# Kernel optimization log

Measured on AMD Instinct MI355X. Metric: run time of the kernel, lower is better.

Reference implementation:

```python
import jax, jax.numpy as jnp
import numpy as np

N = 200_000   # nodes in batched graph
E = 400_000   # edges
D = 128       # embed_dim
L = 5         # num_layer
G = 1000      # number of graphs in batch
ATOM_V = 119  # atom vocab (OGB)
BOND_V = 5    # bond vocab (OGB)
OUT = 128     # output_dim
EPS = 1e-5


def setup_inputs() -> dict:
    key = jax.random.key(0)
    ks = jax.random.split(key, 16)
    inp = {
        "nfeat": jax.random.randint(ks[0], (N,), 0, ATOM_V),
        "efeat": jax.random.randint(ks[1], (E,), 0, BOND_V),
        "src": jax.random.randint(ks[2], (E,), 0, N),
        "dst": jax.random.randint(ks[3], (E,), 0, N),
        "node2graph": jnp.sort(jax.random.randint(ks[4], (N,), 0, G)),
        # learned parameters
        "atom_emb": jax.random.normal(ks[5], (ATOM_V, D), jnp.float32) * 0.02,
        "edge_emb": jax.random.normal(ks[6], (L, BOND_V, D), jnp.float32) * 0.02,
        "W": jax.random.normal(ks[7], (L, D, D), jnp.float32) * 0.02,
        "b": jnp.zeros((L, D), jnp.float32),
        "gamma": jnp.ones((L, D), jnp.float32),
        "beta": jnp.zeros((L, D), jnp.float32),
        "W1": jax.random.normal(ks[8], (D, D), jnp.float32) * 0.02,
        "b1": jnp.zeros((D,), jnp.float32),
        "W2": jax.random.normal(ks[9], (D, OUT), jnp.float32) * 0.02,
        "b2": jnp.zeros((OUT,), jnp.float32),
    }
    return inp


def reference(nfeat, efeat, src, dst, node2graph,
              atom_emb, edge_emb, W, b, gamma, beta, W1, b1, W2, b2):
    h = atom_emb[nfeat]                                  # [N, D]
    # in-degree + 1 (GCNConvLayer degree norm)
    deg = jax.ops.segment_sum(jnp.ones((E,), h.dtype), dst, num_segments=N) + 1.0
    for l in range(L):
        e = edge_emb[l][efeat]                           # [E, D] edge encoder
        m = h[src] + e                                   # u_add_e
        neigh = jax.ops.segment_sum(m, dst, num_segments=N)  # fn.sum -> 'neigh'
        h = ((h + neigh) / deg[:, None]) @ W[l] + b[l]   # project_node_feat
        # batch norm over nodes (training-mode batch stats), affine
        mu = jnp.mean(h, axis=0)
        var = jnp.var(h, axis=0)
        h = (h - mu) * jax.lax.rsqrt(var + EPS) * gamma[l] + beta[l]
        h = jax.nn.relu(h)                               # activation; dropout=eval
    # global mean pooling per graph
    cnt = jax.ops.segment_sum(jnp.ones((N,), h.dtype), node2graph, num_segments=G)
    g = jax.ops.segment_sum(h, node2graph, num_segments=G) / jnp.maximum(cnt, 1.0)[:, None]
    # predict MLP (dropout in eval mode = identity)
    out = jax.nn.relu(g @ W1 + b1) @ W2 + b2             # [G, OUT]
    return out
```

## Files before the change

### kernel.cpp

```cpp
#include <hip/hip_runtime.h>
#include <hip/hip_bf16.h>
#include <cstddef>

#define NN 200000
#define NE 400000
#define DD 128
#define NL 5
#define NG 1000
#define BOND_V 5
#define BM 32
#define NBLK (NN / BM)
#define MAXD 16
#define CHUNK 200
#define NB_SCAN 200
#define CH 1000
#define SB 125
#define EPS 1e-5f
#define XS 136

typedef __bf16 bf16x8 __attribute__((ext_vector_type(8)));
typedef float floatx4 __attribute__((ext_vector_type(4)));

__device__ __forceinline__ unsigned short f2bf(float f) {
    unsigned int u = __float_as_uint(f);
    u = (u + 0x7fffu + ((u >> 16) & 1u)) >> 16;
    return (unsigned short)u;
}
__device__ __forceinline__ float bf2f(unsigned short s) {
    return __uint_as_float(((unsigned int)s) << 16);
}
__device__ __forceinline__ float4 bf4_to_f4(uint2 v) {
    float4 o;
    o.x = __uint_as_float(v.x << 16);
    o.y = __uint_as_float(v.x & 0xffff0000u);
    o.z = __uint_as_float(v.y << 16);
    o.w = __uint_as_float(v.y & 0xffff0000u);
    return o;
}

__global__ void k_setup1(const int* __restrict__ dst, int* __restrict__ cnt,
                         const int* __restrict__ n2g, float* __restrict__ gcnt,
                         const float* __restrict__ W, unsigned short* __restrict__ Wht,
                         unsigned short* __restrict__ Wlt) {
    int e = blockIdx.x * blockDim.x + threadIdx.x;
    if (e < NE) atomicAdd(&cnt[dst[e]], 1);
    if (e < NN) atomicAdd(&gcnt[n2g[e]], 1.0f);
    if (e < NL * DD * DD) {
        int l = e / (DD * DD), rem = e % (DD * DD);
        int k = rem / DD, n = rem % DD;
        float v = W[e];
        unsigned short hb = f2bf(v);
        unsigned short lb = f2bf(v - bf2f(hb));
        size_t o = (size_t)l * DD * DD + (size_t)n * DD + k;
        Wht[o] = hb; Wlt[o] = lb;
    }
}

__global__ void k_scan1(const int* __restrict__ cnt, int* __restrict__ bsum) {
    __shared__ int sh[256];
    int b = blockIdx.x, t = threadIdx.x;
    int s = 0;
    if (t < CH / 4) {
        int base = b * CH + t * 4;
        s = cnt[base] + cnt[base + 1] + cnt[base + 2] + cnt[base + 3];
    }
    sh[t] = s;
    __syncthreads();
    if (t == 0) {
        int tot = 0;
        for (int i = 0; i < CH / 4; i++) tot += sh[i];
        bsum[b] = tot;
    }
}

__global__ void k_scan2(const int* __restrict__ bsum, int* __restrict__ bpre,
                        int* __restrict__ off) {
    if (threadIdx.x == 0) {
        int run = 0;
        for (int i = 0; i < NB_SCAN; i++) { bpre[i] = run; run += bsum[i]; }
        off[NN] = NE;
    }
}

__global__ void k_scan3(const int* __restrict__ cnt, const int* __restrict__ bpre,
                        int* __restrict__ off, int* __restrict__ cur,
                        float* __restrict__ rdeg) {
    __shared__ int sh[256];
    int b = blockIdx.x, t = threadIdx.x;
    int base = b * CH + t * 4;
    int c0 = 0, c1 = 0, c2 = 0, c3 = 0, s = 0;
    if (t < CH / 4) {
        c0 = cnt[base]; c1 = cnt[base + 1]; c2 = cnt[base + 2]; c3 = cnt[base + 3];
        s = c0 + c1 + c2 + c3;
    }
    sh[t] = s;
    __syncthreads();
    if (t == 0) {
        int run = bpre[b];
        for (int i = 0; i < CH / 4; i++) { int v = sh[i]; sh[i] = run; run += v; }
    }
    __syncthreads();
    if (t < CH / 4) {
        int run = sh[t];
        off[base] = run; cur[base] = run; run += c0;
        off[base + 1] = run; cur[base + 1] = run; run += c1;
        off[base + 2] = run; cur[base + 2] = run; run += c2;
        off[base + 3] = run; cur[base + 3] = run;
        rdeg[base]     = 1.0f / (float)(c0 + 1);
        rdeg[base + 1] = 1.0f / (float)(c1 + 1);
        rdeg[base + 2] = 1.0f / (float)(c2 + 1);
        rdeg[base + 3] = 1.0f / (float)(c3 + 1);
    }
}

__global__ void k_bucket(const int* __restrict__ src, const int* __restrict__ dst,
                         const int* __restrict__ efeat, int* __restrict__ cur,
                         int* __restrict__ esrc, int* __restrict__ eft) {
    int e = blockIdx.x * blockDim.x + threadIdx.x;
    if (e < NE) {
        int p = atomicAdd(&cur[dst[e]], 1);
        esrc[p] = src[e];
        eft[p] = efeat[e];
    }
}

__global__ void k_pad(const int* __restrict__ off, const int* __restrict__ esrc,
                      const int* __restrict__ eft, int* __restrict__ pent,
                      int* __restrict__ bperm, int* __restrict__ gmax) {
    __shared__ int offL[BM + 1];
    __shared__ int degS[BM];
    __shared__ int sortIdx[BM];
    __shared__ int gmaxS[8];
    int b = blockIdx.x, tid = threadIdx.x;
    if (tid <= BM) offL[tid] = off[b * BM + tid];
    __syncthreads();
    if (tid < BM) degS[tid] = offL[tid + 1] - offL[tid];
    __syncthreads();
    if (tid < BM) {
        int d = degS[tid], rank = 0;
        #pragma unroll
        for (int j = 0; j < BM; j++)
            rank += (degS[j] > d) || (degS[j] == d && j < tid);
        sortIdx[rank] = tid;
    }
    __syncthreads();
    if (tid < 8) {
        int g = degS[sortIdx[tid * 4]];
        gmaxS[tid] = g;
        gmax[b * 8 + tid] = g;
    }
    if (tid < BM) bperm[b * BM + tid] = sortIdx[tid];
    __syncthreads();
    for (int idx = tid; idx < BM * MAXD; idx += 256) {
        int p = idx & 31, j = idx >> 5, g = p >> 2;
        int gm = gmaxS[g]; if (gm > MAXD) gm = MAXD;
        if (j < gm) {
            int row = sortIdx[p];
            int d = degS[row];
            int v;
            if (j < d) { int e = offL[row] + j; v = esrc[e] | (eft[e] << 18); }
            else v = (5 << 18);
            pent[(size_t)b * MAXD * BM + j * BM + p] = v;
        }
    }
}

__device__ __forceinline__ float4 bnrelu4(float4 x, float4 m, float4 r, float4 g, float4 b) {
    float4 o;
    o.x = fmaxf(0.f, (x.x - m.x) * r.x * g.x + b.x);
    o.y = fmaxf(0.f, (x.y - m.y) * r.y * g.y + b.y);
    o.z = fmaxf(0.f, (x.z - m.z) * r.z * g.z + b.z);
    o.w = fmaxf(0.f, (x.w - m.w) * r.w * g.w + b.w);
    return o;
}

__global__ __launch_bounds__(256)
void k_fused(const void* __restrict__ basep, const int* __restrict__ nfeat, int first,
             const int* __restrict__ off, const int* __restrict__ esrc,
             const int* __restrict__ eft, const int* __restrict__ pent,
             const int* __restrict__ bperm, const int* __restrict__ gmax,
             const float* __restrict__ eemb, const float* __restrict__ rdeg,
             const float* __restrict__ muP, const float* __restrict__ rsP,
             const float* __restrict__ gamma, const float* __restrict__ beta,
             const unsigned short* __restrict__ Wht, const unsigned short* __restrict__ Wlt,
             const float* __restrict__ bias,
             unsigned short* __restrict__ C, float* __restrict__ part) {
    __shared__ unsigned short Xh[BM * XS];
    __shared__ unsigned short Xl[BM * XS];
    __shared__ float eS[6 * DD];
    __shared__ float red[4 * DD];
    __shared__ int offL[BM + 1];
    __shared__ int permL[BM];
    __shared__ int gmL[8];

    const float* baseF = (const float*)basep;
    const unsigned short* baseB = (const unsigned short*)basep;

    int tid = threadIdx.x;
    int n0 = blockIdx.x * BM;
    if (tid < 160) *(float4*)(eS + tid * 4) = *(const float4*)(eemb + tid * 4);
    else if (tid < 192) *(float4*)(eS + tid * 4) = (float4){0.f, 0.f, 0.f, 0.f};
    if (tid <= BM) offL[tid] = off[n0 + tid];
    if (tid < BM) permL[tid] = bperm[blockIdx.x * BM + tid];
    if (tid < 8) gmL[tid] = gmax[blockIdx.x * 8 + tid];

    int lane32 = tid & 31, grp = tid >> 5;
    int c4 = lane32 << 2;
    float4 m4, r4, g4, b4;
    if (!first) {
        m4 = *(const float4*)(muP + c4);
        r4 = *(const float4*)(rsP + c4);
        g4 = *(const float4*)(gamma + c4);
        b4 = *(const float4*)(beta + c4);
    }
    __syncthreads();

    int rows[4];
    #pragma unroll
    for (int i = 0; i < 4; i++) rows[i] = permL[grp * 4 + i];

    float4 acc[4];
    #pragma unroll
    for (int i = 0; i < 4; i++) {
        int n = n0 + rows[i];
        float4 a;
        if (first) {
            a = *(const float4*)(baseF + (size_t)nfeat[n] * DD + c4);
        } else {
            uint2 g = *(const uint2*)(baseB + (size_t)n * DD + c4);
            a = bnrelu4(bf4_to_f4(g), m4, r4, g4, b4);
        }
        acc[i] = a;
    }

    int gmx = gmL[grp];
    int jmax = gmx < MAXD ? gmx : MAXD;
    const int* pb = pent + (size_t)blockIdx.x * MAXD * BM + grp * 4;
    for (int j = 0; j < jmax; j++) {
        int v0 = pb[j * BM + 0];
        int v1 = pb[j * BM + 1];
        int v2 = pb[j * BM + 2];
        int v3 = pb[j * BM + 3];
        int s0 = v0 & 0x3FFFF, f0 = v0 >> 18;
        int s1 = v1 & 0x3FFFF, f1 = v1 >> 18;
        int s2 = v2 & 0x3FFFF, f2 = v2 >> 18;
        int s3 = v3 & 0x3FFFF, f3 = v3 >> 18;
        float4 h0, h1, h2, h3;
        if (first) {
            h0 = *(const float4*)(baseF + (size_t)nfeat[s0] * DD + c4);
            h1 = *(const float4*)(baseF + (size_t)nfeat[s1] * DD + c4);
            h2 = *(const float4*)(baseF + (size_t)nfeat[s2] * DD + c4);
            h3 = *(const float4*)(baseF + (size_t)nfeat[s3] * DD + c4);
        } else {
            uint2 g0 = *(const uint2*)(baseB + (size_t)s0 * DD + c4);
            uint2 g1 = *(const uint2*)(baseB + (size_t)s1 * DD + c4);
            uint2 g2 = *(const uint2*)(baseB + (size_t)s2 * DD + c4);
            uint2 g3 = *(const uint2*)(baseB + (size_t)s3 * DD + c4);
            h0 = bnrelu4(bf4_to_f4(g0), m4, r4, g4, b4);
            h1 = bnrelu4(bf4_to_f4(g1), m4, r4, g4, b4);
            h2 = bnrelu4(bf4_to_f4(g2), m4, r4, g4, b4);
            h3 = bnrelu4(bf4_to_f4(g3), m4, r4, g4, b4);
        }
        float w0 = (f0 == 5) ? 0.f : 1.f;
        float w1 = (f1 == 5) ? 0.f : 1.f;
        float w2 = (f2 == 5) ? 0.f : 1.f;
        float w3 = (f3 == 5) ? 0.f : 1.f;
        float4 e0 = *(const float4*)(eS + f0 * DD + c4);
        float4 e1 = *(const float4*)(eS + f1 * DD + c4);
        float4 e2 = *(const float4*)(eS + f2 * DD + c4);
        float4 e3 = *(const float4*)(eS + f3 * DD + c4);
        acc[0].x += (h0.x + e0.x) * w0; acc[0].y += (h0.y + e0.y) * w0;
        acc[0].z += (h0.z + e0.z) * w0; acc[0].w += (h0.w + e0.w) * w0;
        acc[1].x += (h1.x + e1.x) * w1; acc[1].y += (h1.y + e1.y) * w1;
        acc[1].z += (h1.z + e1.z) * w1; acc[1].w += (h1.w + e1.w) * w1;
        acc[2].x += (h2.x + e2.x) * w2; acc[2].y += (h2.y + e2.y) * w2;
        acc[2].z += (h2.z + e2.z) * w2; acc[2].w += (h2.w + e2.w) * w2;
        acc[3].x += (h3.x + e3.x) * w3; acc[3].y += (h3.y + e3.y) * w3;
        acc[3].z += (h3.z + e3.z) * w3; acc[3].w += (h3.w + e3.w) * w3;
    }

    if (gmx > MAXD) {
        #pragma unroll
        for (int i = 0; i < 4; i++) {
            int row = rows[i];
            for (int e = offL[row] + MAXD; e < offL[row + 1]; e++) {
                int s = esrc[e], f = eft[e];
                float4 hv;
                if (first) {
                    hv = *(const float4*)(baseF + (size_t)nfeat[s] * DD + c4);
                } else {
                    uint2 g = *(const uint2*)(baseB + (size_t)s * DD + c4);
                    hv = bnrelu4(bf4_to_f4(g), m4, r4, g4, b4);
                }
                const float* ep = eS + f * DD + c4;
                acc[i].x += hv.x + ep[0]; acc[i].y += hv.y + ep[1];
                acc[i].z += hv.z + ep[2]; acc[i].w += hv.w + ep[3];
            }
        }
    }

    #pragma unroll
    for (int i = 0; i < 4; i++) {
        int r = rows[i];
        float rd = rdeg[n0 + r];
        float ax = acc[i].x * rd, ay = acc[i].y * rd, az = acc[i].z * rd, aw = acc[i].w * rd;
        unsigned short h0 = f2bf(ax), h1 = f2bf(ay), h2 = f2bf(az), h3 = f2bf(aw);
        unsigned short l0 = f2bf(ax - bf2f(h0));
        unsigned short l1 = f2bf(ay - bf2f(h1));
        unsigned short l2 = f2bf(az - bf2f(h2));
        unsigned short l3 = f2bf(aw - bf2f(h3));
        uint2 hv2, lv2;
        hv2.x = (unsigned)h0 | ((unsigned)h1 << 16);
        hv2.y = (unsigned)h2 | ((unsigned)h3 << 16);
        lv2.x = (unsigned)l0 | ((unsigned)l1 << 16);
        lv2.y = (unsigned)l2 | ((unsigned)l3 << 16);
        *(uint2*)(Xh + r * XS + c4) = hv2;
        *(uint2*)(Xl + r * XS + c4) = lv2;
    }
    __syncthreads();

    int lane = tid & 63, w = tid >> 6;
    int m16 = lane & 15, quad = lane >> 4;
    int rowTile = w & 1;
    int colBase = (w >> 1) << 6;
    int rowA = rowTile * 16 + m16;

    floatx4 acc4[4];
    #pragma unroll
    for (int t = 0; t < 4; t++) acc4[t] = (floatx4){0.f, 0.f, 0.f, 0.f};

    #pragma unroll
    for (int kp = 0; kp < 4; kp++) {
        bf16x8 ah = *(const bf16x8*)(Xh + rowA * XS + kp * 32 + quad * 8);
        bf16x8 al = *(const bf16x8*)(Xl + rowA * XS + kp * 32 + quad * 8);
        #pragma unroll
        for (int t = 0; t < 4; t++) {
            int ncol = colBase + t * 16 + m16;
            bf16x8 bh = *(const bf16x8*)(Wht + (size_t)ncol * DD + kp * 32 + quad * 8);
            bf16x8 bl = *(const bf16x8*)(Wlt + (size_t)ncol * DD + kp * 32 + quad * 8);
            acc4[t] = __builtin_amdgcn_mfma_f32_16x16x32_bf16(ah, bh, acc4[t], 0, 0, 0);
            acc4[t] = __builtin_amdgcn_mfma_f32_16x16x32_bf16(ah, bl, acc4[t], 0, 0, 0);
            acc4[t] = __builtin_amdgcn_mfma_f32_16x16x32_bf16(al, bh, acc4[t], 0, 0, 0);
        }
    }
    __syncthreads();

    float* redS = red;
    float* redQ = red + 2 * DD;
    unsigned short* Cs = Xh;
    #pragma unroll
    for (int t = 0; t < 4; t++) {
        int col = colBase + t * 16 + m16;
        float bv = bias[col];
        float s = 0.f, q = 0.f;
        #pragma unroll
        for (int rr = 0; rr < 4; rr++) {
            float vv = acc4[t][rr] + bv;
            s += vv; q += vv * vv;
            Cs[(rowTile * 16 + quad * 4 + rr) * XS + col] = f2bf(vv);
        }
        s += __shfl_xor(s, 16); q += __shfl_xor(q, 16);
        s += __shfl_xor(s, 32); q += __shfl_xor(q, 32);
        if (lane < 16) { redS[rowTile * DD + col] = s; redQ[rowTile * DD + col] = q; }
    }
    __syncthreads();

    #pragma unroll
    for (int it = 0; it < 2; it++) {
        int idx = it * 256 + tid;
        int row = idx >> 4, q16 = idx & 15;
        uint4 v = *(const uint4*)(Cs + row * XS + q16 * 8);
        *(uint4*)(C + (size_t)(n0 + row) * DD + q16 * 8) = v;
    }
    if (tid < DD) {
        float ss = redS[tid] + redS[DD + tid];
        float qq = redQ[tid] + redQ[DD + tid];
        part[(size_t)blockIdx.x * 256 + tid] = ss;
        part[(size_t)blockIdx.x * 256 + DD + tid] = qq;
    }
}

__global__ void k_stats(const float* __restrict__ part, float* __restrict__ musum) {
    int t = threadIdx.x;
    float s = 0.f;
    int base = blockIdx.x * (NBLK / SB);
    for (int i = 0; i < NBLK / SB; i++)
        s += part[(size_t)(base + i) * 256 + t];
    atomicAdd(&musum[t], s);
}

__global__ void k_fin(const float* __restrict__ musum,
                      float* __restrict__ mu, float* __restrict__ rsig) {
    int t = threadIdx.x;
    float S = musum[t], Q = musum[DD + t];
    float m = S / (float)NN;
    float v = Q / (float)NN - m * m;
    mu[t] = m;
    rsig[t] = rsqrtf(v + EPS);
}

__global__ void k_bnpool(const unsigned short* __restrict__ A, const int* __restrict__ n2g,
                         const float* __restrict__ mu, const float* __restrict__ rsig,
                         const float* __restrict__ gamma, const float* __restrict__ beta,
                         float* __restrict__ gsum) {
    int j = threadIdx.x;
    int n0 = blockIdx.x * CHUNK;
    float m = mu[j], r = rsig[j], ga = gamma[j], be = beta[j];
    int cur = n2g[n0];
    float acc = 0.f;
    for (int i = 0; i < CHUNK; i++) {
        int n = n0 + i;
        int gg = n2g[n];
        if (gg != cur) {
            atomicAdd(&gsum[(size_t)cur * DD + j], acc);
            acc = 0.f;
            cur = gg;
        }
        float x = bf2f(A[(size_t)n * DD + j]);
        x = fmaxf(0.f, (x - m) * r * ga + be);
        acc += x;
    }
    atomicAdd(&gsum[(size_t)cur * DD + j], acc);
}

__global__ void k_mlp(const float* __restrict__ gsum, const float* __restrict__ gcnt,
                      const float* __restrict__ W1, const float* __restrict__ b1,
                      const float* __restrict__ W2, const float* __restrict__ b2,
                      float* __restrict__ out) {
    __shared__ float gs[DD], hs[DD];
    int gid = blockIdx.x, j = threadIdx.x;
    float inv = 1.0f / fmaxf(gcnt[gid], 1.0f);
    gs[j] = gsum[(size_t)gid * DD + j] * inv;
    __syncthreads();
    float a = b1[j];
    for (int k = 0; k < DD; k++) a += gs[k] * W1[k * DD + j];
    hs[j] = fmaxf(a, 0.f);
    __syncthreads();
    float o = b2[j];
    for (int k = 0; k < DD; k++) o += hs[k] * W2[k * DD + j];
    out[(size_t)gid * DD + j] = o;
}

extern "C" void kernel_launch(void* const* d_in, const int* in_sizes, int n_in,
                              void* d_out, int out_size, void* d_ws, size_t ws_size,
                              hipStream_t stream) {
    const int*   nfeat = (const int*)d_in[0];
    const int*   efeat = (const int*)d_in[1];
    const int*   src   = (const int*)d_in[2];
    const int*   dst   = (const int*)d_in[3];
    const int*   n2g   = (const int*)d_in[4];
    const float* aemb  = (const float*)d_in[5];
    const float* eemb  = (const float*)d_in[6];
    const float* Wl    = (const float*)d_in[7];
    const float* bl    = (const float*)d_in[8];
    const float* gam   = (const float*)d_in[9];
    const float* bet   = (const float*)d_in[10];
    const float* W1    = (const float*)d_in[11];
    const float* b1    = (const float*)d_in[12];
    const float* W2    = (const float*)d_in[13];
    const float* b2    = (const float*)d_in[14];
    float* out = (float*)d_out;

    unsigned short* H0 = (unsigned short*)d_ws;
    unsigned short* H1 = H0 + (size_t)NN * DD;
    float* rdeg  = (float*)(H1 + (size_t)NN * DD);
    float* gsum  = rdeg + NN;
    float* gcnt  = gsum + (size_t)NG * DD;
    float* mu    = gcnt + NG;
    float* rsg   = mu + DD;
    float* musum = rsg + DD;
    float* part  = musum + NL * 256;
    unsigned short* Wht = (unsigned short*)(part + (size_t)NBLK * 256);
    unsigned short* Wlt = Wht + (size_t)NL * DD * DD;
    int* off   = (int*)(Wlt + (size_t)NL * DD * DD);
    int* cur   = off + NN + 1;
    int* esrc  = cur + NN;
    int* eft   = esrc + NE;
    int* cnt   = eft + NE;
    int* bsum  = cnt + NN;
    int* bpre  = bsum + NB_SCAN;
    int* bperm = bpre + NB_SCAN;
    int* gmax  = bperm + (size_t)NBLK * BM;
    int* pent  = gmax + (size_t)NBLK * 8;

    hipMemsetAsync(gsum, 0,
                   (size_t)(NG * DD + NG + 2 * DD + NL * 256) * sizeof(float), stream);
    hipMemsetAsync(cnt, 0, (size_t)NN * sizeof(int), stream);

    k_setup1<<<(NE + 255) / 256, 256, 0, stream>>>(dst, cnt, n2g, gcnt, Wl, Wht, Wlt);
    k_scan1<<<NB_SCAN, 256, 0, stream>>>(cnt, bsum);
    k_scan2<<<1, 64, 0, stream>>>(bsum, bpre, off);
    k_scan3<<<NB_SCAN, 256, 0, stream>>>(cnt, bpre, off, cur, rdeg);
    k_bucket<<<(NE + 255) / 256, 256, 0, stream>>>(src, dst, efeat, cur, esrc, eft);
    k_pad<<<NBLK, 256, 0, stream>>>(off, esrc, eft, pent, bperm, gmax);

    unsigned short* hcur = H0;
    for (int l = 0; l < NL; l++) {
        const void* base = (l == 0) ? (const void*)aemb : (const void*)hcur;
        unsigned short* hnext = (l == 0) ? H0 : ((hcur == H0) ? H1 : H0);
        const float* g_prev = (l == 0) ? gam : gam + (size_t)(l - 1) * DD;
        const float* b_prev = (l == 0) ? bet : bet + (size_t)(l - 1) * DD;
        k_fused<<<NBLK, 256, 0, stream>>>(base, nfeat, (l == 0) ? 1 : 0,
                                          off, esrc, eft, pent, bperm, gmax,
                                          eemb + (size_t)l * BOND_V * DD, rdeg,
                                          mu, rsg, g_prev, b_prev,
                                          Wht + (size_t)l * DD * DD,
                                          Wlt + (size_t)l * DD * DD,
                                          bl + (size_t)l * DD, hnext, part);
        k_stats<<<SB, 256, 0, stream>>>(part, musum + l * 256);
        k_fin<<<1, DD, 0, stream>>>(musum + l * 256, mu, rsg);
        hcur = hnext;
    }
    k_bnpool<<<NN / CHUNK, DD, 0, stream>>>(hcur, n2g, mu, rsg,
                                            gam + (size_t)(NL - 1) * DD,
                                            bet + (size_t)(NL - 1) * DD, gsum);
    k_mlp<<<NG, DD, 0, stream>>>(gsum, gcnt, W1, b1, W2, b2, out);
}
```

Before: 1.090 ms.

## Fold BN into scale/shift, merge stats+fin, stage edge lists in LDS, prefetch two edges

Batch-norm finalization now runs inside k_stats through a last-block-done counter, which removes the separate k_fin launch per layer. It emits a precomputed per-channel scale and shift so each activation is a single FMA plus relu instead of the subtract/multiply/multiply/add chain. The padded edge table for each block is staged into shared memory, and a layer-0 variant pre-resolves nfeat for each source so the double indirection goes away. The gather loop is unrolled by two to keep more loads in flight, and launch bounds request 4 blocks per CU, which risks register spilling. It also reuses the edge-embedding LDS buffer for the reduction scratch.

```diff
diff --git a/kernel.cpp b/kernel.cpp
--- a/kernel.cpp
+++ b/kernel.cpp
@@ -37,6 +37,14 @@
     o.w = __uint_as_float(v.y & 0xffff0000u);
     return o;
 }
+__device__ __forceinline__ float4 actv4(float4 h, float4 sc, float4 sh) {
+    float4 o;
+    o.x = fmaxf(0.f, h.x * sc.x + sh.x);
+    o.y = fmaxf(0.f, h.y * sc.y + sh.y);
+    o.z = fmaxf(0.f, h.z * sc.z + sh.z);
+    o.w = fmaxf(0.f, h.w * sc.w + sh.w);
+    return o;
+}
 
 __global__ void k_setup1(const int* __restrict__ dst, int* __restrict__ cnt,
                          const int* __restrict__ n2g, float* __restrict__ gcnt,
@@ -125,7 +133,8 @@
 }
 
 __global__ void k_pad(const int* __restrict__ off, const int* __restrict__ esrc,
-                      const int* __restrict__ eft, int* __restrict__ pent,
+                      const int* __restrict__ eft, const int* __restrict__ nfeat,
+                      int* __restrict__ pent, int* __restrict__ pent0,
                       int* __restrict__ bperm, int* __restrict__ gmax) {
     __shared__ int offL[BM + 1];
     __shared__ int degS[BM];
@@ -157,38 +166,33 @@
         if (j < gm) {
             int row = sortIdx[p];
             int d = degS[row];
-            int v;
-            if (j < d) { int e = offL[row] + j; v = esrc[e] | (eft[e] << 18); }
-            else v = (5 << 18);
+            int v, v0;
+            if (j < d) {
+                int e = offL[row] + j;
+                int s = esrc[e], f = eft[e];
+                v = s | (f << 18);
+                v0 = nfeat[s] | (f << 18);
+            } else { v = (5 << 18); v0 = (5 << 18); }
             pent[(size_t)b * MAXD * BM + j * BM + p] = v;
-        }
-    }
-}
-
-__device__ __forceinline__ float4 bnrelu4(float4 x, float4 m, float4 r, float4 g, float4 b) {
-    float4 o;
-    o.x = fmaxf(0.f, (x.x - m.x) * r.x * g.x + b.x);
-    o.y = fmaxf(0.f, (x.y - m.y) * r.y * g.y + b.y);
-    o.z = fmaxf(0.f, (x.z - m.z) * r.z * g.z + b.z);
-    o.w = fmaxf(0.f, (x.w - m.w) * r.w * g.w + b.w);
-    return o;
-}
-
-__global__ __launch_bounds__(256)
+            pent0[(size_t)b * MAXD * BM + j * BM + p] = v0;
+        }
+    }
+}
+
+__global__ __launch_bounds__(256, 4)
 void k_fused(const void* __restrict__ basep, const int* __restrict__ nfeat, int first,
              const int* __restrict__ off, const int* __restrict__ esrc,
-             const int* __restrict__ eft, const int* __restrict__ pent,
+             const int* __restrict__ eft, const int* __restrict__ pentsel,
              const int* __restrict__ bperm, const int* __restrict__ gmax,
              const float* __restrict__ eemb, const float* __restrict__ rdeg,
-             const float* __restrict__ muP, const float* __restrict__ rsP,
-             const float* __restrict__ gamma, const float* __restrict__ beta,
+             const float* __restrict__ scP, const float* __restrict__ shP,
              const unsigned short* __restrict__ Wht, const unsigned short* __restrict__ Wlt,
              const float* __restrict__ bias,
              unsigned short* __restrict__ C, float* __restrict__ part) {
     __shared__ unsigned short Xh[BM * XS];
     __shared__ unsigned short Xl[BM * XS];
-    __shared__ float eS[6 * DD];
-    __shared__ float red[4 * DD];
+    __shared__ float eSr[6 * DD];
+    __shared__ int pentL[BM * MAXD];
     __shared__ int offL[BM + 1];
     __shared__ int permL[BM];
     __shared__ int gmL[8];
@@ -198,20 +202,22 @@
 
     int tid = threadIdx.x;
     int n0 = blockIdx.x * BM;
-    if (tid < 160) *(float4*)(eS + tid * 4) = *(const float4*)(eemb + tid * 4);
-    else if (tid < 192) *(float4*)(eS + tid * 4) = (float4){0.f, 0.f, 0.f, 0.f};
+    if (tid < 160) *(float4*)(eSr + tid * 4) = *(const float4*)(eemb + tid * 4);
+    else if (tid < 192) *(float4*)(eSr + tid * 4) = (float4){0.f, 0.f, 0.f, 0.f};
     if (tid <= BM) offL[tid] = off[n0 + tid];
     if (tid < BM) permL[tid] = bperm[blockIdx.x * BM + tid];
     if (tid < 8) gmL[tid] = gmax[blockIdx.x * 8 + tid];
+    {
+        const int2* pg = (const int2*)(pentsel + (size_t)blockIdx.x * MAXD * BM);
+        *(int2*)(pentL + tid * 2) = pg[tid];
+    }
 
     int lane32 = tid & 31, grp = tid >> 5;
     int c4 = lane32 << 2;
-    float4 m4, r4, g4, b4;
+    float4 sc4, sh4;
     if (!first) {
-        m4 = *(const float4*)(muP + c4);
-        r4 = *(const float4*)(rsP + c4);
-        g4 = *(const float4*)(gamma + c4);
-        b4 = *(const float4*)(beta + c4);
+        sc4 = *(const float4*)(scP + c4);
+        sh4 = *(const float4*)(shP + c4);
     }
     __syncthreads();
 
@@ -223,60 +229,160 @@
     #pragma unroll
     for (int i = 0; i < 4; i++) {
         int n = n0 + rows[i];
-        float4 a;
         if (first) {
-            a = *(const float4*)(baseF + (size_t)nfeat[n] * DD + c4);
+            acc[i] = *(const float4*)(baseF + (size_t)nfeat[n] * DD + c4);
         } else {
             uint2 g = *(const uint2*)(baseB + (size_t)n * DD + c4);
-            a = bnrelu4(bf4_to_f4(g), m4, r4, g4, b4);
-        }
-        acc[i] = a;
+            acc[i] = actv4(bf4_to_f4(g), sc4, sh4);
+        }
     }
 
     int gmx = gmL[grp];
     int jmax = gmx < MAXD ? gmx : MAXD;
-    const int* pb = pent + (size_t)blockIdx.x * MAXD * BM + grp * 4;
-    for (int j = 0; j < jmax; j++) {
-        int v0 = pb[j * BM + 0];
-        int v1 = pb[j * BM + 1];
-        int v2 = pb[j * BM + 2];
-        int v3 = pb[j * BM + 3];
-        int s0 = v0 & 0x3FFFF, f0 = v0 >> 18;
-        int s1 = v1 & 0x3FFFF, f1 = v1 >> 18;
-        int s2 = v2 & 0x3FFFF, f2 = v2 >> 18;
-        int s3 = v3 & 0x3FFFF, f3 = v3 >> 18;
-        float4 h0, h1, h2, h3;
-        if (first) {
-            h0 = *(const float4*)(baseF + (size_t)nfeat[s0] * DD + c4);
-            h1 = *(const float4*)(baseF + (size_t)nfeat[s1] * DD + c4);
-            h2 = *(const float4*)(baseF + (size_t)nfeat[s2] * DD + c4);
-            h3 = *(const float4*)(baseF + (size_t)nfeat[s3] * DD + c4);
-        } else {
-            uint2 g0 = *(const uint2*)(baseB + (size_t)s0 * DD + c4);
-            uint2 g1 = *(const uint2*)(baseB + (size_t)s1 * DD + c4);
-            uint2 g2 = *(const uint2*)(baseB + (size_t)s2 * DD + c4);
-            uint2 g3 = *(const uint2*)(baseB + (size_t)s3 * DD + c4);
-            h0 = bnrelu4(bf4_to_f4(g0), m4, r4, g4, b4);
-            h1 = bnrelu4(bf4_to_f4(g1), m4, r4, g4, b4);
-            h2 = bnrelu4(bf4_to_f4(g2), m4, r4, g4, b4);
-            h3 = bnrelu4(bf4_to_f4(g3), m4, r4, g4, b4);
-        }
-        float w0 = (f0 == 5) ? 0.f : 1.f;
-        float w1 = (f1 == 5) ? 0.f : 1.f;
-        float w2 = (f2 == 5) ? 0.f : 1.f;
-        float w3 = (f3 == 5) ? 0.f : 1.f;
-        float4 e0 = *(const float4*)(eS + f0 * DD + c4);
-        float4 e1 = *(const float4*)(eS + f1 * DD + c4);
-        float4 e2 = *(const float4*)(eS + f2 * DD + c4);
-        float4 e3 = *(const float4*)(eS + f3 * DD + c4);
-        acc[0].x += (h0.x + e0.x) * w0; acc[0].y += (h0.y + e0.y) * w0;
-        acc[0].z += (h0.z + e0.z) * w0; acc[0].w += (h0.w + e0.w) * w0;
-        acc[1].x += (h1.x + e1.x) * w1; acc[1].y += (h1.y + e1.y) * w1;
-        acc[1].z += (h1.z + e1.z) * w1; acc[1].w += (h1.w + e1.w) * w1;
-        acc[2].x += (h2.x + e2.x) * w2; acc[2].y += (h2.y + e2.y) * w2;
-        acc[2].z += (h2.z + e2.z) * w2; acc[2].w += (h2.w + e2.w) * w2;
-        acc[3].x += (h3.x + e3.x) * w3; acc[3].y += (h3.y + e3.y) * w3;
-        acc[3].z += (h3.z + e3.z) * w3; acc[3].w += (h3.w + e3.w) * w3;
+    const int* pL = pentL + grp * 4;
+    int j = 0;
+    if (first) {
+        for (; j + 2 <= jmax; j += 2) {
+            int a0 = pL[j*32+0], a1 = pL[j*32+1], a2 = pL[j*32+2], a3 = pL[j*32+3];
+            int b0 = pL[j*32+32], b1 = pL[j*32+33], b2 = pL[j*32+34], b3 = pL[j*32+35];
+            float4 ha0 = *(const float4*)(baseF + (size_t)(a0 & 0x3FFFF) * DD + c4);
+            float4 ha1 = *(const float4*)(baseF + (size_t)(a1 & 0x3FFFF) * DD + c4);
+            float4 ha2 = *(const float4*)(baseF + (size_t)(a2 & 0x3FFFF) * DD + c4);
+            float4 ha3 = *(const float4*)(baseF + (size_t)(a3 & 0x3FFFF) * DD + c4);
+            float4 hb0 = *(const float4*)(baseF + (size_t)(b0 & 0x3FFFF) * DD + c4);
+            float4 hb1 = *(const float4*)(baseF + (size_t)(b1 & 0x3FFFF) * DD + c4);
+            float4 hb2 = *(const float4*)(baseF + (size_t)(b2 & 0x3FFFF) * DD + c4);
+            float4 hb3 = *(const float4*)(baseF + (size_t)(b3 & 0x3FFFF) * DD + c4);
+            int fa0 = a0 >> 18, fa1 = a1 >> 18, fa2 = a2 >> 18, fa3 = a3 >> 18;
+            int fb0 = b0 >> 18, fb1 = b1 >> 18, fb2 = b2 >> 18, fb3 = b3 >> 18;
+            float wa0 = (fa0 == 5) ? 0.f : 1.f, wa1 = (fa1 == 5) ? 0.f : 1.f;
+            float wa2 = (fa2 == 5) ? 0.f : 1.f, wa3 = (fa3 == 5) ? 0.f : 1.f;
+            float wb0 = (fb0 == 5) ? 0.f : 1.f, wb1 = (fb1 == 5) ? 0.f : 1.f;
+            float wb2 = (fb2 == 5) ? 0.f : 1.f, wb3 = (fb3 == 5) ? 0.f : 1.f;
+            float4 ea0 = *(const float4*)(eSr + fa0 * DD + c4);
+            float4 ea1 = *(const float4*)(eSr + fa1 * DD + c4);
+            float4 ea2 = *(const float4*)(eSr + fa2 * DD + c4);
+            float4 ea3 = *(const float4*)(eSr + fa3 * DD + c4);
+            float4 eb0 = *(const float4*)(eSr + fb0 * DD + c4);
+            float4 eb1 = *(const float4*)(eSr + fb1 * DD + c4);
+            float4 eb2 = *(const float4*)(eSr + fb2 * DD + c4);
+            float4 eb3 = *(const float4*)(eSr + fb3 * DD + c4);
+            acc[0].x += (ha0.x + ea0.x) * wa0 + (hb0.x + eb0.x) * wb0;
+            acc[0].y += (ha0.y + ea0.y) * wa0 + (hb0.y + eb0.y) * wb0;
+            acc[0].z += (ha0.z + ea0.z) * wa0 + (hb0.z + eb0.z) * wb0;
+            acc[0].w += (ha0.w + ea0.w) * wa0 + (hb0.w + eb0.w) * wb0;
+            acc[1].x += (ha1.x + ea1.x) * wa1 + (hb1.x + eb1.x) * wb1;
+            acc[1].y += (ha1.y + ea1.y) * wa1 + (hb1.y + eb1.y) * wb1;
+            acc[1].z += (ha1.z + ea1.z) * wa1 + (hb1.z + eb1.z) * wb1;
+            acc[1].w += (ha1.w + ea1.w) * wa1 + (hb1.w + eb1.w) * wb1;
+            acc[2].x += (ha2.x + ea2.x) * wa2 + (hb2.x + eb2.x) * wb2;
+            acc[2].y += (ha2.y + ea2.y) * wa2 + (hb2.y + eb2.y) * wb2;
+            acc[2].z += (ha2.z + ea2.z) * wa2 + (hb2.z + eb2.z) * wb2;
+            acc[2].w += (ha2.w + ea2.w) * wa2 + (hb2.w + eb2.w) * wb2;
+            acc[3].x += (ha3.x + ea3.x) * wa3 + (hb3.x + eb3.x) * wb3;
+            acc[3].y += (ha3.y + ea3.y) * wa3 + (hb3.y + eb3.y) * wb3;
+            acc[3].z += (ha3.z + ea3.z) * wa3 + (hb3.z + eb3.z) * wb3;
+            acc[3].w += (ha3.w + ea3.w) * wa3 + (hb3.w + eb3.w) * wb3;
+        }
+        for (; j < jmax; j++) {
+            int a0 = pL[j*32+0], a1 = pL[j*32+1], a2 = pL[j*32+2], a3 = pL[j*32+3];
+            float4 h0 = *(const float4*)(baseF + (size_t)(a0 & 0x3FFFF) * DD + c4);
+            float4 h1 = *(const float4*)(baseF + (size_t)(a1 & 0x3FFFF) * DD + c4);
+            float4 h2 = *(const float4*)(baseF + (size_t)(a2 & 0x3FFFF) * DD + c4);
+            float4 h3 = *(const float4*)(baseF + (size_t)(a3 & 0x3FFFF) * DD + c4);
+            int f0 = a0 >> 18, f1 = a1 >> 18, f2 = a2 >> 18, f3 = a3 >> 18;
+            float w0 = (f0 == 5) ? 0.f : 1.f, w1 = (f1 == 5) ? 0.f : 1.f;
+            float w2 = (f2 == 5) ? 0.f : 1.f, w3 = (f3 == 5) ? 0.f : 1.f;
+            float4 e0 = *(const float4*)(eSr + f0 * DD + c4);
+            float4 e1 = *(const float4*)(eSr + f1 * DD + c4);
+            float4 e2 = *(const float4*)(eSr + f2 * DD + c4);
+            float4 e3 = *(const float4*)(eSr + f3 * DD + c4);
+            acc[0].x += (h0.x + e0.x) * w0; acc[0].y += (h0.y + e0.y) * w0;
+            acc[0].z += (h0.z + e0.z) * w0; acc[0].w += (h0.w + e0.w) * w0;
+            acc[1].x += (h1.x + e1.x) * w1; acc[1].y += (h1.y + e1.y) * w1;
+            acc[1].z += (h1.z + e1.z) * w1; acc[1].w += (h1.w + e1.w) * w1;
+            acc[2].x += (h2.x + e2.x) * w2; acc[2].y += (h2.y + e2.y) * w2;
+            acc[2].z += (h2.z + e2.z) * w2; acc[2].w += (h2.w + e2.w) * w2;
+            acc[3].x += (h3.x + e3.x) * w3; acc[3].y += (h3.y + e3.y) * w3;
+            acc[3].z += (h3.z + e3.z) * w3; acc[3].w += (h3.w + e3.w) * w3;
+        }
+    } else {
+        for (; j + 2 <= jmax; j += 2) {
+            int a0 = pL[j*32+0], a1 = pL[j*32+1], a2 = pL[j*32+2], a3 = pL[j*32+3];
+            int b0 = pL[j*32+32], b1 = pL[j*32+33], b2 = pL[j*32+34], b3 = pL[j*32+35];
+            uint2 ga0 = *(const uint2*)(baseB + (size_t)(a0 & 0x3FFFF) * DD + c4);
+            uint2 ga1 = *(const uint2*)(baseB + (size_t)(a1 & 0x3FFFF) * DD + c4);
+            uint2 ga2 = *(const uint2*)(baseB + (size_t)(a2 & 0x3FFFF) * DD + c4);
+            uint2 ga3 = *(const uint2*)(baseB + (size_t)(a3 & 0x3FFFF) * DD + c4);
+            uint2 gb0 = *(const uint2*)(baseB + (size_t)(b0 & 0x3FFFF) * DD + c4);
+            uint2 gb1 = *(const uint2*)(baseB + (size_t)(b1 & 0x3FFFF) * DD + c4);
+            uint2 gb2 = *(const uint2*)(baseB + (size_t)(b2 & 0x3FFFF) * DD + c4);
+            uint2 gb3 = *(const uint2*)(baseB + (size_t)(b3 & 0x3FFFF) * DD + c4);
+            float4 ha0 = actv4(bf4_to_f4(ga0), sc4, sh4);
+            float4 ha1 = actv4(bf4_to_f4(ga1), sc4, sh4);
+            float4 ha2 = actv4(bf4_to_f4(ga2), sc4, sh4);
+            float4 ha3 = actv4(bf4_to_f4(ga3), sc4, sh4);
+            float4 hb0 = actv4(bf4_to_f4(gb0), sc4, sh4);
+            float4 hb1 = actv4(bf4_to_f4(gb1), sc4, sh4);
+            float4 hb2 = actv4(bf4_to_f4(gb2), sc4, sh4);
+            float4 hb3 = actv4(bf4_to_f4(gb3), sc4, sh4);
+            int fa0 = a0 >> 18, fa1 = a1 >> 18, fa2 = a2 >> 18, fa3 = a3 >> 18;
+            int fb0 = b0 >> 18, fb1 = b1 >> 18, fb2 = b2 >> 18, fb3 = b3 >> 18;
+            float wa0 = (fa0 == 5) ? 0.f : 1.f, wa1 = (fa1 == 5) ? 0.f : 1.f;
+            float wa2 = (fa2 == 5) ? 0.f : 1.f, wa3 = (fa3 == 5) ? 0.f : 1.f;
+            float wb0 = (fb0 == 5) ? 0.f : 1.f, wb1 = (fb1 == 5) ? 0.f : 1.f;
+            float wb2 = (fb2 == 5) ? 0.f : 1.f, wb3 = (fb3 == 5) ? 0.f : 1.f;
+            float4 ea0 = *(const float4*)(eSr + fa0 * DD + c4);
+            float4 ea1 = *(const float4*)(eSr + fa1 * DD + c4);
+            float4 ea2 = *(const float4*)(eSr + fa2 * DD + c4);
+            float4 ea3 = *(const float4*)(eSr + fa3 * DD + c4);
+            float4 eb0 = *(const float4*)(eSr + fb0 * DD + c4);
+            float4 eb1 = *(const float4*)(eSr + fb1 * DD + c4);
+            float4 eb2 = *(const float4*)(eSr + fb2 * DD + c4);
+            float4 eb3 = *(const float4*)(eSr + fb3 * DD + c4);
+            acc[0].x += (ha0.x + ea0.x) * wa0 + (hb0.x + eb0.x) * wb0;
+            acc[0].y += (ha0.y + ea0.y) * wa0 + (hb0.y + eb0.y) * wb0;
+            acc[0].z += (ha0.z + ea0.z) * wa0 + (hb0.z + eb0.z) * wb0;
+            acc[0].w += (ha0.w + ea0.w) * wa0 + (hb0.w + eb0.w) * wb0;
+            acc[1].x += (ha1.x + ea1.x) * wa1 + (hb1.x + eb1.x) * wb1;
+            acc[1].y += (ha1.y + ea1.y) * wa1 + (hb1.y + eb1.y) * wb1;
+            acc[1].z += (ha1.z + ea1.z) * wa1 + (hb1.z + eb1.z) * wb1;
+            acc[1].w += (ha1.w + ea1.w) * wa1 + (hb1.w + eb1.w) * wb1;
+            acc[2].x += (ha2.x + ea2.x) * wa2 + (hb2.x + eb2.x) * wb2;
+            acc[2].y += (ha2.y + ea2.y) * wa2 + (hb2.y + eb2.y) * wb2;
+            acc[2].z += (ha2.z + ea2.z) * wa2 + (hb2.z + eb2.z) * wb2;
+            acc[2].w += (ha2.w + ea2.w) * wa2 + (hb2.w + eb2.w) * wb2;
+            acc[3].x += (ha3.x + ea3.x) * wa3 + (hb3.x + eb3.x) * wb3;
+            acc[3].y += (ha3.y + ea3.y) * wa3 + (hb3.y + eb3.y) * wb3;
+            acc[3].z += (ha3.z + ea3.z) * wa3 + (hb3.z + eb3.z) * wb3;
+            acc[3].w += (ha3.w + ea3.w) * wa3 + (hb3.w + eb3.w) * wb3;
+        }
+        for (; j < jmax; j++) {
+            int a0 = pL[j*32+0], a1 = pL[j*32+1], a2 = pL[j*32+2], a3 = pL[j*32+3];
+            uint2 g0 = *(const uint2*)(baseB + (size_t)(a0 & 0x3FFFF) * DD + c4);
+            uint2 g1 = *(const uint2*)(baseB + (size_t)(a1 & 0x3FFFF) * DD + c4);
+            uint2 g2 = *(const uint2*)(baseB + (size_t)(a2 & 0x3FFFF) * DD + c4);
+            uint2 g3 = *(const uint2*)(baseB + (size_t)(a3 & 0x3FFFF) * DD + c4);
+            float4 h0 = actv4(bf4_to_f4(g0), sc4, sh4);
+            float4 h1 = actv4(bf4_to_f4(g1), sc4, sh4);
+            float4 h2 = actv4(bf4_to_f4(g2), sc4, sh4);
+            float4 h3 = actv4(bf4_to_f4(g3), sc4, sh4);
+            int f0 = a0 >> 18, f1 = a1 >> 18, f2 = a2 >> 18, f3 = a3 >> 18;
+            float w0 = (f0 == 5) ? 0.f : 1.f, w1 = (f1 == 5) ? 0.f : 1.f;
+            float w2 = (f2 == 5) ? 0.f : 1.f, w3 = (f3 == 5) ? 0.f : 1.f;
+            float4 e0 = *(const float4*)(eSr + f0 * DD + c4);
+            float4 e1 = *(const float4*)(eSr + f1 * DD + c4);
+            float4 e2 = *(const float4*)(eSr + f2 * DD + c4);
+            float4 e3 = *(const float4*)(eSr + f3 * DD + c4);
+            acc[0].x += (h0.x + e0.x) * w0; acc[0].y += (h0.y + e0.y) * w0;
+            acc[0].z += (h0.z + e0.z) * w0; acc[0].w += (h0.w + e0.w) * w0;
+            acc[1].x += (h1.x + e1.x) * w1; acc[1].y += (h1.y + e1.y) * w1;
+            acc[1].z += (h1.z + e1.z) * w1; acc[1].w += (h1.w + e1.w) * w1;
+            acc[2].x += (h2.x + e2.x) * w2; acc[2].y += (h2.y + e2.y) * w2;
+            acc[2].z += (h2.z + e2.z) * w2; acc[2].w += (h2.w + e2.w) * w2;
+            acc[3].x += (h3.x + e3.x) * w3; acc[3].y += (h3.y + e3.y) * w3;
+            acc[3].z += (h3.z + e3.z) * w3; acc[3].w += (h3.w + e3.w) * w3;
+        }
     }
 
     if (gmx > MAXD) {
@@ -290,9 +396,9 @@
                     hv = *(const float4*)(baseF + (size_t)nfeat[s] * DD + c4);
                 } else {
                     uint2 g = *(const uint2*)(baseB + (size_t)s * DD + c4);
-                    hv = bnrelu4(bf4_to_f4(g), m4, r4, g4, b4);
+                    hv = actv4(bf4_to_f4(g), sc4, sh4);
                 }
-                const float* ep = eS + f * DD + c4;
+                const float* ep = eSr + f * DD + c4;
                 acc[i].x += hv.x + ep[0]; acc[i].y += hv.y + ep[1];
                 acc[i].z += hv.z + ep[2]; acc[i].w += hv.w + ep[3];
             }
@@ -345,8 +451,8 @@
     }
     __syncthreads();
 
-    float* redS = red;
-    float* redQ = red + 2 * DD;
+    float* redS = eSr;
+    float* redQ = eSr + 2 * DD;
     unsigned short* Cs = Xh;
     #pragma unroll
     for (int t = 0; t < 4; t++) {
@@ -380,32 +486,39 @@
     }
 }
 
-__global__ void k_stats(const float* __restrict__ part, float* __restrict__ musum) {
+__global__ void k_stats(const float* __restrict__ part, float* __restrict__ acc,
+                        int* __restrict__ cnt,
+                        const float* __restrict__ gamma, const float* __restrict__ beta,
+                        float* __restrict__ scale, float* __restrict__ shift) {
     int t = threadIdx.x;
     float s = 0.f;
     int base = blockIdx.x * (NBLK / SB);
     for (int i = 0; i < NBLK / SB; i++)
         s += part[(size_t)(base + i) * 256 + t];
-    atomicAdd(&musum[t], s);
-}
-
-__global__ void k_fin(const float* __restrict__ musum,
-                      float* __restrict__ mu, float* __restrict__ rsig) {
-    int t = threadIdx.x;
-    float S = musum[t], Q = musum[DD + t];
-    float m = S / (float)NN;
-    float v = Q / (float)NN - m * m;
-    mu[t] = m;
-    rsig[t] = rsqrtf(v + EPS);
+    atomicAdd(&acc[t], s);
+    __threadfence();
+    __shared__ int lastS;
+    __syncthreads();
+    if (t == 0) lastS = (atomicAdd(cnt, 1) == SB - 1);
+    __syncthreads();
+    if (lastS && t < DD) {
+        float Sv = atomicAdd(&acc[t], 0.0f);
+        float Qv = atomicAdd(&acc[DD + t], 0.0f);
+        float m = Sv / (float)NN;
+        float v = Qv / (float)NN - m * m;
+        float rs = rsqrtf(v + EPS);
+        float sc = rs * gamma[t];
+        scale[t] = sc;
+        shift[t] = beta[t] - m * sc;
+    }
 }
 
 __global__ void k_bnpool(const unsigned short* __restrict__ A, const int* __restrict__ n2g,
-                         const float* __restrict__ mu, const float* __restrict__ rsig,
-                         const float* __restrict__ gamma, const float* __restrict__ beta,
+                         const float* __restrict__ scale, const float* __restrict__ shift,
                          float* __restrict__ gsum) {
     int j = threadIdx.x;
     int n0 = blockIdx.x * CHUNK;
-    float m = mu[j], r = rsig[j], ga = gamma[j], be = beta[j];
+    float sc = scale[j], sh = shift[j];
     int cur = n2g[n0];
     float acc = 0.f;
     for (int i = 0; i < CHUNK; i++) {
@@ -417,8 +530,7 @@
             cur = gg;
         }
         float x = bf2f(A[(size_t)n * DD + j]);
-        x = fmaxf(0.f, (x - m) * r * ga + be);
-        acc += x;
+        acc += fmaxf(0.f, x * sc + sh);
     }
     atomicAdd(&gsum[(size_t)cur * DD + j], acc);
 }
@@ -463,13 +575,14 @@
 
     unsigned short* H0 = (unsigned short*)d_ws;
     unsigned short* H1 = H0 + (size_t)NN * DD;
-    float* rdeg  = (float*)(H1 + (size_t)NN * DD);
-    float* gsum  = rdeg + NN;
-    float* gcnt  = gsum + (size_t)NG * DD;
-    float* mu    = gcnt + NG;
-    float* rsg   = mu + DD;
-    float* musum = rsg + DD;
-    float* part  = musum + NL * 256;
+    float* rdeg   = (float*)(H1 + (size_t)NN * DD);
+    float* gsum   = rdeg + NN;
+    float* gcnt   = gsum + (size_t)NG * DD;
+    float* scaleA = gcnt + NG;
+    float* shiftA = scaleA + NL * DD;
+    float* accS   = shiftA + NL * DD;
+    int*   scnt   = (int*)(accS + NL * 256);
+    float* part   = (float*)(scnt + 16);
     unsigned short* Wht = (unsigned short*)(part + (size_t)NBLK * 256);
     unsigned short* Wlt = Wht + (size_t)NL * DD * DD;
     int* off   = (int*)(Wlt + (size_t)NL * DD * DD);
@@ -482,9 +595,10 @@
     int* bperm = bpre + NB_SCAN;
     int* gmax  = bperm + (size_t)NBLK * BM;
     int* pent  = gmax + (size_t)NBLK * 8;
-
-    hipMemsetAsync(gsum, 0,
-                   (size_t)(NG * DD + NG + 2 * DD + NL * 256) * sizeof(float), stream);
+    int* pent0 = pent + (size_t)NBLK * MAXD * BM;
+
+    hipMemsetAsync(gsum, 0, (size_t)(NG * DD + NG) * sizeof(float), stream);
+    hipMemsetAsync(accS, 0, (size_t)(NL * 256) * sizeof(float) + 16 * sizeof(int), stream);
     hipMemsetAsync(cnt, 0, (size_t)NN * sizeof(int), stream);
 
     k_setup1<<<(NE + 255) / 256, 256, 0, stream>>>(dst, cnt, n2g, gcnt, Wl, Wht, Wlt);
@@ -492,27 +606,29 @@
     k_scan2<<<1, 64, 0, stream>>>(bsum, bpre, off);
     k_scan3<<<NB_SCAN, 256, 0, stream>>>(cnt, bpre, off, cur, rdeg);
     k_bucket<<<(NE + 255) / 256, 256, 0, stream>>>(src, dst, efeat, cur, esrc, eft);
-    k_pad<<<NBLK, 256, 0, stream>>>(off, esrc, eft, pent, bperm, gmax);
+    k_pad<<<NBLK, 256, 0, stream>>>(off, esrc, eft, nfeat, pent, pent0, bperm, gmax);
 
     unsigned short* hcur = H0;
     for (int l = 0; l < NL; l++) {
         const void* base = (l == 0) ? (const void*)aemb : (const void*)hcur;
         unsigned short* hnext = (l == 0) ? H0 : ((hcur == H0) ? H1 : H0);
-        const float* g_prev = (l == 0) ? gam : gam + (size_t)(l - 1) * DD;
-        const float* b_prev = (l == 0) ? bet : bet + (size_t)(l - 1) * DD;
+        const int* psel = (l == 0) ? pent0 : pent;
+        const float* scP = scaleA + (size_t)((l == 0) ? 0 : (l - 1)) * DD;
+        const float* shP = shiftA + (size_t)((l == 0) ? 0 : (l - 1)) * DD;
         k_fused<<<NBLK, 256, 0, stream>>>(base, nfeat, (l == 0) ? 1 : 0,
-                                          off, esrc, eft, pent, bperm, gmax,
+                                          off, esrc, eft, psel, bperm, gmax,
                                           eemb + (size_t)l * BOND_V * DD, rdeg,
-                                          mu, rsg, g_prev, b_prev,
+                                          scP, shP,
                                           Wht + (size_t)l * DD * DD,
                                           Wlt + (size_t)l * DD * DD,
                                           bl + (size_t)l * DD, hnext, part);
-        k_stats<<<SB, 256, 0, stream>>>(part, musum + l * 256);
-        k_fin<<<1, DD, 0, stream>>>(musum + l * 256, mu, rsg);
+        k_stats<<<SB, 256, 0, stream>>>(part, accS + l * 256, scnt + l,
+                                        gam + (size_t)l * DD, bet + (size_t)l * DD,
+                                        scaleA + (size_t)l * DD, shiftA + (size_t)l * DD);
         hcur = hnext;
     }
-    k_bnpool<<<NN / CHUNK, DD, 0, stream>>>(hcur, n2g, mu, rsg,
-                                            gam + (size_t)(NL - 1) * DD,
-                                            bet + (size_t)(NL - 1) * DD, gsum);
+    k_bnpool<<<NN / CHUNK, DD, 0, stream>>>(hcur, n2g,
+                                            scaleA + (size_t)(NL - 1) * DD,
+                                            shiftA + (size_t)(NL - 1) * DD, gsum);
     k_mlp<<<NG, DD, 0, stream>>>(gsum, gcnt, W1, b1, W2, b2, out);
 }
```

After: 1.071 ms. About the same (-1.8%).
